# Performance work log

Hardware: AMD Instinct MI355X
Metric: run time of the kernel (lower is better)

The kernel has to match this reference:

```python
import jax, jax.numpy as jnp
import numpy as np

B, H, W, EMB = 8, 32, 32, 768
N_HEADS, HEAD = 12, 64
RATIO = 4
EPS = 1e-5


def layer_norm(x, g, b):
    m = jnp.mean(x, axis=-1, keepdims=True)
    v = jnp.var(x, axis=-1, keepdims=True)
    return (x - m) * jax.lax.rsqrt(v + EPS) * g + b


def block(x, g, b, W1, b1, W2, b2):
    # Block(in, out, ratio): LayerNorm -> Linear(in, in*ratio) -> GELU -> Linear(in*ratio, out)
    y = layer_norm(x, g, b)
    y = jax.nn.gelu(y @ W1 + b1, approximate=False)
    return y @ W2 + b2


def _mk_block_params(key, d_in, d_out, ratio=RATIO):
    hid = int(d_in * ratio)
    k1, k2 = jax.random.split(key)
    return (
        jnp.ones((d_in,), jnp.float32),            # ln gamma
        jnp.zeros((d_in,), jnp.float32),           # ln beta
        jax.random.normal(k1, (d_in, hid), jnp.float32) * 0.02,
        jnp.zeros((hid,), jnp.float32),
        jax.random.normal(k2, (hid, d_out), jnp.float32) * 0.02,
        jnp.zeros((d_out,), jnp.float32),
    )


def setup_inputs() -> dict:
    key = jax.random.key(0)
    kx, kq, kp, km = jax.random.split(key, 4)
    x = jax.random.normal(kx, (B, H, W, EMB), jnp.float32)
    qkv = _mk_block_params(kq, EMB, 3 * N_HEADS * HEAD)
    proj = _mk_block_params(kp, N_HEADS * HEAD, EMB)
    mlp = _mk_block_params(km, EMB, EMB)
    names = ["g", "b", "W1", "b1", "W2", "b2"]
    out = {"x": x}
    for pre, p in (("qkv", qkv), ("proj", proj), ("mlp", mlp)):
        for n, v in zip(names, p):
            out[f"{pre}_{n}"] = v
    return out


def reference(x, qkv_g, qkv_b, qkv_W1, qkv_b1, qkv_W2, qkv_b2,
              proj_g, proj_b, proj_W1, proj_b1, proj_W2, proj_b2,
              mlp_g, mlp_b, mlp_W1, mlp_b1, mlp_W2, mlp_b2):
    b, h, w, c = x.shape
    seq = h * w
    scale = 1.0 / HEAD ** 0.5

    t = block(x, qkv_g, qkv_b, qkv_W1, qkv_b1, qkv_W2, qkv_b2)  # (b,h,w,3*n*s)
    # Rearrange 'b h w (k n s) -> k (b n) (h w) s'
    t = t.reshape(b, seq, 3, N_HEADS, HEAD).transpose(2, 0, 3, 1, 4)
    t = t.reshape(3, b * N_HEADS, seq, HEAD)
    q, k, v = t[0], t[1], t[2]

    score = jnp.einsum('btc,blc->btl', q, k)          # (b*n, seq, seq)
    attn = jax.nn.softmax(score * scale, axis=2)
    out = jnp.einsum('btc,btl->blc', v, attn)          # (b*n, seq, head) -- attn^T @ v, as in source

    # Rearrange '(b n) (h w) s -> b h w (n s)'
    out = out.reshape(b, N_HEADS, h, w, HEAD).transpose(0, 2, 3, 1, 4)
    out = out.reshape(b, h, w, N_HEADS * HEAD)

    y = block(out, proj_g, proj_b, proj_W1, proj_b1, proj_W2, proj_b2)
    y = block(y, mlp_g, mlp_b, mlp_W1, mlp_b1, mlp_W2, mlp_b2)
    return y
```

## Files before the change

### kernel.cpp

```cpp
#include <hip/hip_runtime.h>
#include <stdint.h>


typedef unsigned short u16;
typedef __attribute__((ext_vector_type(8))) short bf16x8;
typedef __attribute__((ext_vector_type(4))) float f32x4;
typedef __attribute__((address_space(1))) unsigned int as1_u32;
typedef __attribute__((address_space(3))) unsigned int as3_u32;

#define PHALF 6291456

__device__ __forceinline__ float bf2f(u16 u) {
  union { unsigned int i; float f; } v; v.i = ((unsigned int)u) << 16; return v.f;
}
__device__ __forceinline__ u16 f2bf(float f) {
  union { float f; unsigned int i; } v; v.f = f;
  unsigned int r = v.i + 0x7fffu + ((v.i >> 16) & 1u);
  return (u16)(r >> 16);
}
__device__ __forceinline__ float gelu_exact(float x) {
  return 0.5f * x * (1.0f + erff(x * 0.70710678118654752f));
}
__device__ __forceinline__ void async_ld16(const u16* g, u16* l) {
  __builtin_amdgcn_global_load_lds((const as1_u32*)g, (as3_u32*)l, 16, 0, 0);
}

__global__ __launch_bounds__(256) void ln_kernel(const void* __restrict__ xv,
                                                 const float* __restrict__ g,
                                                 const float* __restrict__ be,
                                                 u16* __restrict__ out, int inMode) {
  int token = blockIdx.x, tid = threadIdx.x;
  int wave = tid >> 6, lane = tid & 63;
  float v0, v1, v2;
  if (inMode == 1) {
    const float* row = (const float*)xv + (size_t)token * 768;
    v0 = row[tid]; v1 = row[tid + 256]; v2 = row[tid + 512];
  } else if (inMode == 2) {
    const float* row = (const float*)xv + (size_t)token * 768;
    const float* row2 = row + PHALF;
    v0 = row[tid] + row2[tid];
    v1 = row[tid + 256] + row2[tid + 256];
    v2 = row[tid + 512] + row2[tid + 512];
  } else {
    const u16* row = (const u16*)xv + (size_t)token * 768;
    v0 = bf2f(row[tid]); v1 = bf2f(row[tid + 256]); v2 = bf2f(row[tid + 512]);
  }
  float s = v0 + v1 + v2;
  float q = v0 * v0 + v1 * v1 + v2 * v2;
#pragma unroll
  for (int m = 1; m < 64; m <<= 1) { s += __shfl_xor(s, m); q += __shfl_xor(q, m); }
  __shared__ float red[8];
  if (lane == 0) { red[wave] = s; red[4 + wave] = q; }
  __syncthreads();
  s = red[0] + red[1] + red[2] + red[3];
  q = red[4] + red[5] + red[6] + red[7];
  float mean = s * (1.0f / 768.0f);
  float var  = q * (1.0f / 768.0f) - mean * mean;
  float inv  = rsqrtf(var + 1e-5f);
  u16* o = out + (size_t)token * 768;
  o[tid]       = f2bf((v0 - mean) * inv * g[tid]       + be[tid]);
  o[tid + 256] = f2bf((v1 - mean) * inv * g[tid + 256] + be[tid + 256]);
  o[tid + 512] = f2bf((v2 - mean) * inv * g[tid + 512] + be[tid + 512]);
}

__global__ __launch_bounds__(256) void transpose_f32_bf16(const float* __restrict__ in,
                                                          u16* __restrict__ out,
                                                          int R, int Cc) {
  __shared__ u16 tile[32][33];
  int c0 = blockIdx.x * 32, r0 = blockIdx.y * 32;
  int tx = threadIdx.x, ty = threadIdx.y;
  for (int i = ty; i < 32; i += 8)
    tile[i][tx] = f2bf(in[(size_t)(r0 + i) * Cc + c0 + tx]);
  __syncthreads();
  for (int i = ty; i < 32; i += 8)
    out[(size_t)(c0 + i) * R + r0 + tx] = tile[tx][i];
}

__global__ __launch_bounds__(256) void vtrans(const u16* __restrict__ t,
                                              u16* __restrict__ vt) {
  int bh = blockIdx.z, b = bh / 12, h = bh % 12;
  int t0 = blockIdx.x * 32, c0 = blockIdx.y * 32;
  __shared__ u16 tile[32][33];
  int tx = threadIdx.x, ty = threadIdx.y;
  for (int i = ty; i < 32; i += 8)
    tile[i][tx] = t[(size_t)(b * 1024 + t0 + i) * 2304 + 1536 + h * 64 + c0 + tx];
  __syncthreads();
  for (int i = ty; i < 32; i += 8)
    vt[(size_t)bh * 65536 + (size_t)(c0 + i) * 1024 + t0 + tx] = tile[tx][i];
}

__global__ __launch_bounds__(256) void add2_kernel(const float* __restrict__ P,
                                                   float* __restrict__ out) {
  int idx = blockIdx.x * 256 + threadIdx.x;
  const f32x4* p0 = (const f32x4*)P;
  const f32x4* p1 = (const f32x4*)(P + PHALF);
  ((f32x4*)out)[idx] = p0[idx] + p1[idx];
}

#define BM 128
#define BN 128
#define BKK 64

__global__ __launch_bounds__(256, 4) void gemm_mfma(
    const u16* __restrict__ A, int lda,
    const u16* __restrict__ B, int ldb,
    void* __restrict__ C, int ldc,
    int M, int N, int kSplit,
    const float* __restrict__ bias, int act, int cF32, long long cZStride) {
  __shared__ u16 As[BM * BKK];
  __shared__ u16 Bs[BN * BKK];
  int gx = gridDim.x, gy = gridDim.y;
  int bx, by;
  if ((gy & 7) == 0) {
    int lin = blockIdx.y * gx + blockIdx.x;
    int xcd = lin & 7, s = lin >> 3;
    int r = s / gx;
    by = xcd * (gy >> 3) + r;
    bx = s - r * gx;
  } else { bx = blockIdx.x; by = blockIdx.y; }
  int m0 = by * BM, n0 = bx * BN;
  int kOff = blockIdx.z * kSplit;
  int tid = threadIdx.x;
  int wave = tid >> 6, lane = tid & 63;
  int quad = lane >> 4, lo = lane & 15;
  int wr = (wave >> 1) * 64, wc = (wave & 1) * 64;

  f32x4 acc[4][4];
#pragma unroll
  for (int i = 0; i < 4; ++i)
#pragma unroll
    for (int j = 0; j < 4; ++j) acc[i][j] = (f32x4){0.f, 0.f, 0.f, 0.f};

  for (int k0 = kOff; k0 < kOff + kSplit; k0 += BKK) {
#pragma unroll
    for (int p = 0; p < 4; ++p) {
      int idx = tid + p * 256;
      int row = idx >> 3;
      int gch = ((idx & 7) ^ (row & 7)) * 8;
      int ldsOff = (wave * 64 + p * 256) * 8;
      async_ld16(A + (long long)(m0 + row) * lda + k0 + gch, As + ldsOff);
      async_ld16(B + (long long)(n0 + row) * ldb + k0 + gch, Bs + ldsOff);
    }
    __syncthreads();
#pragma unroll
    for (int ks = 0; ks < 2; ++ks) {
      bf16x8 af[4], bf[4];
#pragma unroll
      for (int i = 0; i < 4; ++i) {
        int m = wr + i * 16 + lo;
        int slot = (ks * 4 + quad) ^ (m & 7);
        af[i] = *(const bf16x8*)(As + m * BKK + slot * 8);
      }
#pragma unroll
      for (int j = 0; j < 4; ++j) {
        int n = wc + j * 16 + lo;
        int slot = (ks * 4 + quad) ^ (n & 7);
        bf[j] = *(const bf16x8*)(Bs + n * BKK + slot * 8);
      }
#pragma unroll
      for (int i = 0; i < 4; ++i)
#pragma unroll
        for (int j = 0; j < 4; ++j)
          acc[i][j] = __builtin_amdgcn_mfma_f32_16x16x32_bf16(af[i], bf[j], acc[i][j], 0, 0, 0);
    }
    __syncthreads();
  }

  long long cZ = (long long)blockIdx.z * cZStride;
#pragma unroll
  for (int j = 0; j < 4; ++j) {
    int col = n0 + wc + j * 16 + lo;
    float bv = (bias && blockIdx.z == 0) ? bias[col] : 0.0f;
#pragma unroll
    for (int i = 0; i < 4; ++i) {
      int rb = m0 + wr + i * 16 + quad * 4;
#pragma unroll
      for (int r = 0; r < 4; ++r) {
        int row = rb + r;
        float v = acc[i][j][r] + bv;
        if (act) v = gelu_exact(v);
        long long ci = cZ + (long long)row * ldc + col;
        if (cF32) ((float*)C)[ci] = v;
        else      ((u16*)C)[ci] = f2bf(v);
      }
    }
  }
}

__global__ __launch_bounds__(256, 2) void zstats(const u16* __restrict__ tb,
                                                 float* __restrict__ zinv) {
  int bh = blockIdx.y, b = bh / 12, h = bh % 12;
  int t0 = blockIdx.x * 128;
  __shared__ u16 Qs[128 * 64];
  __shared__ u16 Ks[128 * 64];
  __shared__ float zred[4][128];
  int tid = threadIdx.x, wave = tid >> 6, lane = tid & 63;
  int quad = lane >> 4, lo = lane & 15;
  const u16* qbase = tb + (size_t)(b * 1024) * 2304 + h * 64;
  const u16* kbase = qbase + 768;

#pragma unroll
  for (int p = 0; p < 4; ++p) {
    int idx = tid + p * 256, row = idx >> 3;
    int ch = ((idx & 7) ^ (row & 7)) * 8;
    async_ld16(qbase + (size_t)(t0 + row) * 2304 + ch, Qs + (wave * 64 + p * 256) * 8);
  }
  float zacc[8];
#pragma unroll
  for (int j = 0; j < 8; ++j) zacc[j] = 0.f;

  for (int lt = 0; lt < 8; ++lt) {
#pragma unroll
    for (int p = 0; p < 4; ++p) {
      int idx = tid + p * 256, row = idx >> 3;
      int ch = ((idx & 7) ^ (row & 7)) * 8;
      async_ld16(kbase + (size_t)(lt * 128 + row) * 2304 + ch, Ks + (wave * 64 + p * 256) * 8);
    }
    __syncthreads();
    f32x4 acc[2][8];
#pragma unroll
    for (int i = 0; i < 2; ++i)
#pragma unroll
      for (int j = 0; j < 8; ++j) acc[i][j] = (f32x4){0.f, 0.f, 0.f, 0.f};
#pragma unroll
    for (int ks = 0; ks < 2; ++ks) {
      bf16x8 af[2], bf[8];
#pragma unroll
      for (int i = 0; i < 2; ++i) {
        int m = wave * 32 + i * 16 + lo;
        int slot = (ks * 4 + quad) ^ (m & 7);
        af[i] = *(const bf16x8*)(Ks + m * 64 + slot * 8);
      }
#pragma unroll
      for (int j = 0; j < 8; ++j) {
        int n = j * 16 + lo;
        int slot = (ks * 4 + quad) ^ (n & 7);
        bf[j] = *(const bf16x8*)(Qs + n * 64 + slot * 8);
      }
#pragma unroll
      for (int i = 0; i < 2; ++i)
#pragma unroll
        for (int j = 0; j < 8; ++j)
          acc[i][j] = __builtin_amdgcn_mfma_f32_16x16x32_bf16(af[i], bf[j], acc[i][j], 0, 0, 0);
    }
#pragma unroll
    for (int j = 0; j < 8; ++j)
#pragma unroll
      for (int i = 0; i < 2; ++i)
#pragma unroll
        for (int r = 0; r < 4; ++r)
          zacc[j] += __expf(acc[i][j][r] * 0.125f);
    __syncthreads();
  }
#pragma unroll
  for (int j = 0; j < 8; ++j) {
    float v = zacc[j];
    v += __shfl_xor(v, 16);
    v += __shfl_xor(v, 32);
    zacc[j] = v;
  }
  if (quad == 0)
#pragma unroll
    for (int j = 0; j < 8; ++j) zred[wave][j * 16 + lo] = zacc[j];
  __syncthreads();
  if (tid < 128) {
    float z = zred[0][tid] + zred[1][tid] + zred[2][tid] + zred[3][tid];
    zinv[(size_t)bh * 1024 + t0 + tid] = 1.0f / z;
  }
}

__global__ __launch_bounds__(256, 2) void attn_out(const u16* __restrict__ tb,
                                                   const u16* __restrict__ vt,
                                                   const float* __restrict__ zinv,
                                                   u16* __restrict__ ao) {
  int bh = blockIdx.y, b = bh / 12, h = bh % 12;
  int l0 = blockIdx.x * 128;
  __shared__ u16 Ks[128 * 64];
  __shared__ u16 Qs[64 * 64];
  __shared__ u16 Vs[64 * 64];
  __shared__ u16 Es[128 * 64];
  int tid = threadIdx.x, wave = tid >> 6, lane = tid & 63;
  int quad = lane >> 4, lo = lane & 15;
  const u16* qbase = tb + (size_t)(b * 1024) * 2304 + h * 64;
  const u16* kbase = qbase + 768;
  const u16* vbase = vt + (size_t)bh * 65536;
  const float* zf = zinv + (size_t)bh * 1024;

#pragma unroll
  for (int p = 0; p < 4; ++p) {
    int idx = tid + p * 256, row = idx >> 3;
    int ch = ((idx & 7) ^ (row & 7)) * 8;
    async_ld16(kbase + (size_t)(l0 + row) * 2304 + ch, Ks + (wave * 64 + p * 256) * 8);
  }
  f32x4 oacc[2][4];
#pragma unroll
  for (int i = 0; i < 2; ++i)
#pragma unroll
    for (int j = 0; j < 4; ++j) oacc[i][j] = (f32x4){0.f, 0.f, 0.f, 0.f};

  for (int tt = 0; tt < 16; ++tt) {
    int t0 = tt * 64;
#pragma unroll
    for (int p = 0; p < 2; ++p) {
      int idx = tid + p * 256, row = idx >> 3;
      int ch = ((idx & 7) ^ (row & 7)) * 8;
      async_ld16(qbase + (size_t)(t0 + row) * 2304 + ch, Qs + (wave * 64 + p * 256) * 8);
      async_ld16(vbase + (size_t)row * 1024 + t0 + ch, Vs + (wave * 64 + p * 256) * 8);
    }
    __syncthreads();
    f32x4 sacc[2][4];
#pragma unroll
    for (int i = 0; i < 2; ++i)
#pragma unroll
      for (int j = 0; j < 4; ++j) sacc[i][j] = (f32x4){0.f, 0.f, 0.f, 0.f};
#pragma unroll
    for (int ks = 0; ks < 2; ++ks) {
      bf16x8 af[2], bq[4];
#pragma unroll
      for (int i = 0; i < 2; ++i) {
        int m = wave * 32 + i * 16 + lo;
        int slot = (ks * 4 + quad) ^ (m & 7);
        af[i] = *(const bf16x8*)(Ks + m * 64 + slot * 8);
      }
#pragma unroll
      for (int j = 0; j < 4; ++j) {
        int n = j * 16 + lo;
        int slot = (ks * 4 + quad) ^ (n & 7);
        bq[j] = *(const bf16x8*)(Qs + n * 64 + slot * 8);
      }
#pragma unroll
      for (int i = 0; i < 2; ++i)
#pragma unroll
        for (int j = 0; j < 4; ++j)
          sacc[i][j] = __builtin_amdgcn_mfma_f32_16x16x32_bf16(af[i], bq[j], sacc[i][j], 0, 0, 0);
    }
#pragma unroll
    for (int j = 0; j < 4; ++j) {
      int t_loc = j * 16 + lo;
      float zi = zf[t0 + t_loc];
      int ch = t_loc >> 3, pos = t_loc & 7;
#pragma unroll
      for (int i = 0; i < 2; ++i)
#pragma unroll
        for (int r = 0; r < 4; ++r) {
          int l_loc = wave * 32 + i * 16 + quad * 4 + r;
          float e = __expf(sacc[i][j][r] * 0.125f) * zi;
          Es[l_loc * 64 + ((ch ^ (l_loc & 7)) * 8 + pos)] = f2bf(e);
        }
    }
#pragma unroll
    for (int ks = 0; ks < 2; ++ks) {
      bf16x8 ae[2], bv[4];
#pragma unroll
      for (int i = 0; i < 2; ++i) {
        int m = wave * 32 + i * 16 + lo;
        int slot = (ks * 4 + quad) ^ (m & 7);
        ae[i] = *(const bf16x8*)(Es + m * 64 + slot * 8);
      }
#pragma unroll
      for (int j = 0; j < 4; ++j) {
        int n = j * 16 + lo;
        int slot = (ks * 4 + quad) ^ (n & 7);
        bv[j] = *(const bf16x8*)(Vs + n * 64 + slot * 8);
      }
#pragma unroll
      for (int i = 0; i < 2; ++i)
#pragma unroll
        for (int j = 0; j < 4; ++j)
          oacc[i][j] = __builtin_amdgcn_mfma_f32_16x16x32_bf16(ae[i], bv[j], oacc[i][j], 0, 0, 0);
    }
    __syncthreads();
  }
#pragma unroll
  for (int j = 0; j < 4; ++j) {
    int c = j * 16 + lo;
#pragma unroll
    for (int i = 0; i < 2; ++i)
#pragma unroll
      for (int r = 0; r < 4; ++r) {
        int l = l0 + wave * 32 + i * 16 + quad * 4 + r;
        ao[(size_t)(b * 1024 + l) * 768 + h * 64 + c] = f2bf(oacc[i][j][r]);
      }
  }
}

extern "C" void kernel_launch(void* const* d_in, const int* in_sizes, int n_in,
                              void* d_out, int out_size, void* d_ws, size_t ws_size,
                              hipStream_t stream) {
  const float* x       = (const float*)d_in[0];
  const float* qkv_g   = (const float*)d_in[1];
  const float* qkv_b   = (const float*)d_in[2];
  const float* qkv_W1  = (const float*)d_in[3];
  const float* qkv_b1  = (const float*)d_in[4];
  const float* qkv_W2  = (const float*)d_in[5];
  const float* qkv_b2  = (const float*)d_in[6];
  const float* proj_g  = (const float*)d_in[7];
  const float* proj_b  = (const float*)d_in[8];
  const float* proj_W1 = (const float*)d_in[9];
  const float* proj_b1 = (const float*)d_in[10];
  const float* proj_W2 = (const float*)d_in[11];
  const float* proj_b2 = (const float*)d_in[12];
  const float* mlp_g   = (const float*)d_in[13];
  const float* mlp_b   = (const float*)d_in[14];
  const float* mlp_W1  = (const float*)d_in[15];
  const float* mlp_b1  = (const float*)d_in[16];
  const float* mlp_W2  = (const float*)d_in[17];
  const float* mlp_b2  = (const float*)d_in[18];

  u16* ws  = (u16*)d_ws;
  u16* xn  = ws;
  u16* tb  = ws + 6291456;
  u16* ao  = ws + 25165824;
  u16* yb  = ws + 31457280;
  u16* vt  = ws + 37748736;
  u16* wt1 = ws + 44040192;
  u16* wt2 = ws + 46399488;
  u16* hS  = ws + 53477376;
  float* zinv = (float*)xn;
  float* Pf  = (float*)tb;

  transpose_f32_bf16<<<dim3(96, 24), dim3(32, 8), 0, stream>>>(qkv_W1, wt1, 768, 3072);
  transpose_f32_bf16<<<dim3(72, 96), dim3(32, 8), 0, stream>>>(qkv_W2, wt2, 3072, 2304);
  ln_kernel<<<8192, 256, 0, stream>>>(x, qkv_g, qkv_b, xn, 1);
  gemm_mfma<<<dim3(24, 64), dim3(256), 0, stream>>>(
      xn, 768, wt1, 768, hS, 3072, 8192, 3072, 768, qkv_b1, 1, 0, 0);
  gemm_mfma<<<dim3(18, 64), dim3(256), 0, stream>>>(
      hS, 3072, wt2, 3072, tb, 2304, 8192, 2304, 3072, qkv_b2, 0, 0, 0);

  vtrans<<<dim3(32, 2, 96), dim3(32, 8), 0, stream>>>(tb, vt);
  zstats<<<dim3(8, 96), dim3(256), 0, stream>>>(tb, zinv);
  attn_out<<<dim3(8, 96), dim3(256), 0, stream>>>(tb, vt, zinv, ao);

  transpose_f32_bf16<<<dim3(96, 24), dim3(32, 8), 0, stream>>>(proj_W1, wt1, 768, 3072);
  transpose_f32_bf16<<<dim3(24, 96), dim3(32, 8), 0, stream>>>(proj_W2, wt2, 3072, 768);
  ln_kernel<<<8192, 256, 0, stream>>>(ao, proj_g, proj_b, xn, 0);
  gemm_mfma<<<dim3(24, 64), dim3(256), 0, stream>>>(
      xn, 768, wt1, 768, hS, 3072, 8192, 3072, 768, proj_b1, 1, 0, 0);
  gemm_mfma<<<dim3(6, 64, 2), dim3(256), 0, stream>>>(
      hS, 3072, wt2, 3072, Pf, 768, 8192, 768, 1536, proj_b2, 0, 1, PHALF);

  transpose_f32_bf16<<<dim3(96, 24), dim3(32, 8), 0, stream>>>(mlp_W1, wt1, 768, 3072);
  transpose_f32_bf16<<<dim3(24, 96), dim3(32, 8), 0, stream>>>(mlp_W2, wt2, 3072, 768);
  ln_kernel<<<8192, 256, 0, stream>>>(Pf, mlp_g, mlp_b, xn, 2);
  gemm_mfma<<<dim3(24, 64), dim3(256), 0, stream>>>(
      xn, 768, wt1, 768, hS, 3072, 8192, 3072, 768, mlp_b1, 1, 0, 0);
  gemm_mfma<<<dim3(6, 64, 2), dim3(256), 0, stream>>>(
      hS, 3072, wt2, 3072, Pf, 768, 8192, 768, 1536, mlp_b2, 0, 1, PHALF);
  add2_kernel<<<6144, 256, 0, stream>>>(Pf, (float*)d_out);
}
```

Baseline: 715.0 us.

## Add 256x256-tile 8-wave GEMM with phased prefetch for large projections

Introduces a new bf16 MFMA GEMM kernel with 256x256 output tiles, 512 threads, double-buffered LDS, and a four-phase schedule that interleaves async global-to-LDS loads with MFMA work, using setprio and an XCD-aware block remap. It replaces the older 128-tile GEMM for the three hidden-expansion GEMMs and the QKV output GEMM. The goal is more data reuse per tile and better overlap of loads with compute. In exchange it uses 128KB of LDS and many accumulator registers, launches fewer blocks (which may underfill the GPU), and depends on M and N being multiples of 256.

```diff
diff --git a/kernel.cpp b/kernel.cpp
--- a/kernel.cpp
+++ b/kernel.cpp
@@ -24,6 +24,8 @@
 __device__ __forceinline__ void async_ld16(const u16* g, u16* l) {
   __builtin_amdgcn_global_load_lds((const as1_u32*)g, (as3_u32*)l, 16, 0, 0);
 }
+
+#define BARRIER() do { asm volatile("" ::: "memory"); __builtin_amdgcn_s_barrier(); asm volatile("" ::: "memory"); } while (0)
 
 __global__ __launch_bounds__(256) void ln_kernel(const void* __restrict__ xv,
                                                  const float* __restrict__ g,
@@ -187,6 +189,121 @@
   }
 }
 
+__global__ __launch_bounds__(512, 2) void gemm_256(
+    const u16* __restrict__ A, int lda,
+    const u16* __restrict__ B, int ldb,
+    u16* __restrict__ C, int ldc,
+    int T,
+    const float* __restrict__ bias, int act) {
+  __shared__ u16 As[2][256 * 64];
+  __shared__ u16 Bs[2][256 * 64];
+  int gx = gridDim.x, gy = gridDim.y;
+  int lin = blockIdx.y * gx + blockIdx.x;
+  int xcd = lin & 7, sl = lin >> 3;
+  int rr = sl / gx;
+  int by = xcd * (gy >> 3) + rr;
+  int bx = sl - rr * gx;
+  int m0 = by * 256, n0 = bx * 256;
+  int tid = threadIdx.x;
+  int wv = tid >> 6, lane = tid & 63;
+  int quad = lane >> 4, lo = lane & 15;
+  int wm = (wv >> 2) * 128;
+  int wn = (wv & 3) * 64;
+
+  int srow = tid >> 3;
+  int schunk = tid & 7;
+  int sx = (schunk ^ (srow & 7)) * 8;
+
+#define STG(Xg, ld, base0, Xs, P, h, kt) do {                                 \
+    const u16* g0_ = (Xg) + (long long)((base0) + (h) * 64 + srow) * (ld)     \
+                     + (kt) * 64 + sx;                                         \
+    async_ld16(g0_,                 &Xs[P][(h) * 4096 + wv * 512]);            \
+    async_ld16(g0_ + 128LL * (ld),  &Xs[P][(h) * 4096 + 8192 + wv * 512]);     \
+  } while (0)
+
+  f32x4 acc[8][4];
+#pragma unroll
+  for (int i = 0; i < 8; ++i)
+#pragma unroll
+    for (int j = 0; j < 4; ++j) acc[i][j] = (f32x4){0.f, 0.f, 0.f, 0.f};
+
+  STG(A, lda, m0, As, 0, 0, 0);
+  STG(B, ldb, n0, Bs, 0, 0, 0);
+  STG(A, lda, m0, As, 0, 1, 0);
+  STG(B, ldb, n0, Bs, 0, 1, 0);
+  STG(A, lda, m0, As, 1, 0, 1);
+  STG(B, ldb, n0, Bs, 1, 0, 1);
+  asm volatile("s_waitcnt vmcnt(4)" ::: "memory");
+  BARRIER();
+
+#define PHASE(P, g, e, STAGES, TAILWAIT) do {                                 \
+    bf16x8 af[2][4], bf[2][2];                                                \
+    _Pragma("unroll")                                                          \
+    for (int ks = 0; ks < 2; ++ks) {                                           \
+      _Pragma("unroll")                                                        \
+      for (int i = 0; i < 4; ++i) {                                            \
+        int m_ = wm + (g) * 64 + i * 16 + lo;                                  \
+        af[ks][i] = *(const bf16x8*)(&As[P][m_ * 64 + (((ks * 4 + quad) ^ (m_ & 7)) * 8)]); \
+      }                                                                        \
+      _Pragma("unroll")                                                        \
+      for (int j = 0; j < 2; ++j) {                                            \
+        int n_ = wn + (e) * 32 + j * 16 + lo;                                  \
+        bf[ks][j] = *(const bf16x8*)(&Bs[P][n_ * 64 + (((ks * 4 + quad) ^ (n_ & 7)) * 8)]); \
+      }                                                                        \
+    }                                                                          \
+    STAGES;                                                                    \
+    BARRIER();                                                                 \
+    asm volatile("s_waitcnt lgkmcnt(0)" ::: "memory");                         \
+    __builtin_amdgcn_sched_barrier(0);                                         \
+    __builtin_amdgcn_s_setprio(1);                                             \
+    _Pragma("unroll")                                                          \
+    for (int ks = 0; ks < 2; ++ks)                                             \
+      _Pragma("unroll")                                                        \
+      for (int i = 0; i < 4; ++i)                                              \
+        _Pragma("unroll")                                                      \
+        for (int j = 0; j < 2; ++j)                                            \
+          acc[(g) * 4 + i][(e) * 2 + j] = __builtin_amdgcn_mfma_f32_16x16x32_bf16( \
+              af[ks][i], bf[ks][j], acc[(g) * 4 + i][(e) * 2 + j], 0, 0, 0);   \
+    __builtin_amdgcn_s_setprio(0);                                             \
+    TAILWAIT;                                                                  \
+    BARRIER();                                                                 \
+  } while (0)
+
+  for (int t = 0; t < T; ++t) {
+    int P = t & 1;
+    int tn  = (t + 1 < T) ? t + 1 : T - 1;
+    int tn2 = (t + 2 < T) ? t + 2 : T - 1;
+    PHASE(P, 0, 0, { STG(A, lda, m0, As, P ^ 1, 1, tn); }, );
+    PHASE(P, 0, 1, { STG(B, ldb, n0, Bs, P ^ 1, 1, tn); }, );
+    PHASE(P, 1, 0, { STG(A, lda, m0, As, P, 0, tn2); }, );
+    PHASE(P, 1, 1, { STG(B, ldb, n0, Bs, P, 0, tn2); },
+          asm volatile("s_waitcnt vmcnt(4)" ::: "memory"));
+  }
+  asm volatile("s_waitcnt vmcnt(0)" ::: "memory");
+#undef PHASE
+#undef STG
+
+#pragma unroll
+  for (int g = 0; g < 2; ++g)
+#pragma unroll
+    for (int e = 0; e < 2; ++e)
+#pragma unroll
+      for (int j = 0; j < 2; ++j) {
+        int col = n0 + wn + e * 32 + j * 16 + lo;
+        float bv = bias ? bias[col] : 0.0f;
+#pragma unroll
+        for (int i = 0; i < 4; ++i) {
+          int rb = m0 + wm + g * 64 + i * 16 + quad * 4;
+#pragma unroll
+          for (int r2 = 0; r2 < 4; ++r2) {
+            float v = acc[g * 4 + i][e * 2 + j][r2] + bv;
+            if (act) v = gelu_exact(v);
+            C[(long long)(rb + r2) * ldc + col] = f2bf(v);
+          }
+        }
+      }
+}
+
 __global__ __launch_bounds__(256, 2) void zstats(const u16* __restrict__ tb,
                                                  float* __restrict__ zinv) {
   int bh = blockIdx.y, b = bh / 12, h = bh % 12;
@@ -422,10 +539,10 @@
   transpose_f32_bf16<<<dim3(96, 24), dim3(32, 8), 0, stream>>>(qkv_W1, wt1, 768, 3072);
   transpose_f32_bf16<<<dim3(72, 96), dim3(32, 8), 0, stream>>>(qkv_W2, wt2, 3072, 2304);
   ln_kernel<<<8192, 256, 0, stream>>>(x, qkv_g, qkv_b, xn, 1);
-  gemm_mfma<<<dim3(24, 64), dim3(256), 0, stream>>>(
-      xn, 768, wt1, 768, hS, 3072, 8192, 3072, 768, qkv_b1, 1, 0, 0);
-  gemm_mfma<<<dim3(18, 64), dim3(256), 0, stream>>>(
-      hS, 3072, wt2, 3072, tb, 2304, 8192, 2304, 3072, qkv_b2, 0, 0, 0);
+  gemm_256<<<dim3(12, 32), dim3(512), 0, stream>>>(
+      xn, 768, wt1, 768, hS, 3072, 12, qkv_b1, 1);
+  gemm_256<<<dim3(9, 32), dim3(512), 0, stream>>>(
+      hS, 3072, wt2, 3072, tb, 2304, 48, qkv_b2, 0);
 
   vtrans<<<dim3(32, 2, 96), dim3(32, 8), 0, stream>>>(tb, vt);
   zstats<<<dim3(8, 96), dim3(256), 0, stream>>>(tb, zinv);
@@ -434,16 +551,16 @@
   transpose_f32_bf16<<<dim3(96, 24), dim3(32, 8), 0, stream>>>(proj_W1, wt1, 768, 3072);
   transpose_f32_bf16<<<dim3(24, 96), dim3(32, 8), 0, stream>>>(proj_W2, wt2, 3072, 768);
   ln_kernel<<<8192, 256, 0, stream>>>(ao, proj_g, proj_b, xn, 0);
-  gemm_mfma<<<dim3(24, 64), dim3(256), 0, stream>>>(
-      xn, 768, wt1, 768, hS, 3072, 8192, 3072, 768, proj_b1, 1, 0, 0);
+  gemm_256<<<dim3(12, 32), dim3(512), 0, stream>>>(
+      xn, 768, wt1, 768, hS, 3072, 12, proj_b1, 1);
   gemm_mfma<<<dim3(6, 64, 2), dim3(256), 0, stream>>>(
       hS, 3072, wt2, 3072, Pf, 768, 8192, 768, 1536, proj_b2, 0, 1, PHALF);
 
   transpose_f32_bf16<<<dim3(96, 24), dim3(32, 8), 0, stream>>>(mlp_W1, wt1, 768, 3072);
   transpose_f32_bf16<<<dim3(24, 96), dim3(32, 8), 0, stream>>>(mlp_W2, wt2, 3072, 768);
   ln_kernel<<<8192, 256, 0, stream>>>(Pf, mlp_g, mlp_b, xn, 2);
-  gemm_mfma<<<dim3(24, 64), dim3(256), 0, stream>>>(
-      xn, 768, wt1, 768, hS, 3072, 8192, 3072, 768, mlp_b1, 1, 0, 0);
+  gemm_256<<<dim3(12, 32), dim3(512), 0, stream>>>(
+      xn, 768, wt1, 768, hS, 3072, 12, mlp_b1, 1);
   gemm_mfma<<<dim3(6, 64, 2), dim3(256), 0, stream>>>(
       hS, 3072, wt2, 3072, Pf, 768, 8192, 768, 1536, mlp_b2, 0, 1, PHALF);
   add2_kernel<<<6144, 256, 0, stream>>>(Pf, (float*)d_out);
```

After: 915.8 us. +28.1%, slower.
